# Performance work log

Hardware: AMD Instinct MI355X
Metric: run time of the kernel (lower is better)

Reference implementation:

```python
import jax, jax.numpy as jnp
import numpy as np

B, T, N, C = 32, 12, 1024, 64
NW = T - 3  # number of temporal windows / conv output length


def setup_inputs() -> dict:
    key = jax.random.key(0)
    ks = jax.random.split(key, 10)
    return {
        "data": jax.random.normal(ks[0], (B, T, N, C), jnp.float32),
        "adj": jax.random.uniform(ks[1], (4 * N, 4 * N), jnp.float32) / (4.0 * N),
        "temporal_emb": jax.random.normal(ks[2], (1, T, 1, C), jnp.float32) * 0.05,
        "spatial_emb": jax.random.normal(ks[3], (1, 1, N, C), jnp.float32) * 0.05,
        "conv_wl": jax.random.normal(ks[4], (C, C, 1, 2), jnp.float32) * 0.05,
        "conv_bl": jnp.zeros((C,), jnp.float32),
        "conv_wr": jax.random.normal(ks[5], (C, C, 1, 2), jnp.float32) * 0.05,
        "conv_br": jnp.zeros((C,), jnp.float32),
        "fc_w": jax.random.normal(ks[6], (NW, 3, C, 2 * C), jnp.float32) * 0.05,
        "fc_b": jnp.zeros((NW, 3, 2 * C), jnp.float32),
    }


def reference(data, adj, temporal_emb, spatial_emb, conv_wl, conv_bl, conv_wr, conv_br, fc_w, fc_b):
    Bs, Ts, Ns, Cs = data.shape
    nw = Ts - 3
    x = data + temporal_emb + spatial_emb  # [B,T,N,C]

    # Gated dilated temporal conv: Conv2d kernel (1,2), dilation (1,3) over time
    # out[b,t,n,o] = sum_c w[o,c,0,0]*x[b,t,n,c] + w[o,c,0,1]*x[b,t+3,n,c] + b[o]
    def dconv(w, b):
        return (jnp.einsum('btnc,oc->btno', x[:, :nw], w[:, :, 0, 0])
                + jnp.einsum('btnc,oc->btno', x[:, 3:], w[:, :, 0, 1]) + b)

    data_res = jax.nn.sigmoid(dconv(conv_wl, conv_bl)) * jnp.tanh(dconv(conv_wr, conv_br))  # [B,nw,N,C]

    # Sliding windows of 4 time steps -> [nw, B, 4N, C]
    wins = jnp.stack([x[:, i:i + 4].reshape(Bs, 4 * Ns, Cs) for i in range(nw)], axis=0)

    F = fc_w.shape[-1] // 2  # GLU filter size

    def stsgcm(xw, Ws, bs):
        # xw: [B,4N,C]; Ws: [3,Cin,2F]; bs: [3,2F]
        h = xw
        outs = []
        for k in range(Ws.shape[0]):
            h = jnp.einsum('vw,bwc->bvc', adj, h)       # graph aggregation
            g = h @ Ws[k] + bs[k]                        # linear
            h = g[..., :F] * jax.nn.sigmoid(g[..., F:])  # GLU
            outs.append(h[:, Ns:2 * Ns])                 # middle vertex block
        return jnp.max(jnp.stack(outs, axis=0), axis=0)  # [B,N,F]

    spatial = jax.vmap(stsgcm)(wins, fc_w, fc_b)  # [nw,B,N,F]
    return spatial.transpose(1, 0, 2, 3) + data_res
```

## Files before the change

### kernel.cpp

```cpp
#include <hip/hip_runtime.h>
#include <math.h>

typedef unsigned char  u8;
typedef unsigned short u16;
typedef unsigned int   u32;
typedef __attribute__((ext_vector_type(8))) short bf16x8;
typedef __attribute__((ext_vector_type(4))) float f32x4;

typedef const void __attribute__((address_space(1))) gv1_t;
typedef void       __attribute__((address_space(3))) lv3_t;
#define GLL(g, l) __builtin_amdgcn_global_load_lds((gv1_t*)(g), (lv3_t*)(l), 16, 0, 0)

__device__ __forceinline__ u16 f2b(float x) {
    union { float f; u32 u; } v; v.f = x;
    u32 r = v.u + 0x7FFFu + ((v.u >> 16) & 1u);
    return (u16)(r >> 16);
}
__device__ __forceinline__ float b2f(u32 x) {
    union { u32 u; float f; } v; v.u = x << 16;
    return v.f;
}
__device__ __forceinline__ float fast_sigmoid(float x) {
    return __builtin_amdgcn_rcpf(1.0f + __builtin_amdgcn_exp2f(-x * 1.44269504f));
}
__device__ __forceinline__ float fast_tanh(float x) {
    return 2.0f * __builtin_amdgcn_rcpf(1.0f + __builtin_amdgcn_exp2f(-x * 2.88539008f)) - 1.0f;
}

__device__ __forceinline__ u8 f2e4m3(float x) {
    union { float f; u32 u; } v; v.f = x;
    u32 s = (v.u >> 24) & 0x80u;
    u32 a = v.u & 0x7fffffffu;
    if (a >= 0x43d80000u) return (u8)(s | 0x7e);
    if (a >= 0x3c800000u) {
        u32 expf = a >> 23;
        u32 keep = (a >> 20) & 7u;
        u32 rest = a & 0xfffffu;
        u32 vv = ((expf - 120u) << 3) | keep;
        vv += (rest > 0x80000u) || ((rest == 0x80000u) && (keep & 1u));
        return (u8)(s | vv);
    }
    float t = fabsf(x) * 512.0f;
    u32 ti = (u32)(t + 0.5f);
    return (u8)(s | ti);
}
__device__ __forceinline__ float e4m3f(u32 b) {
    u32 e = (b >> 3) & 15u, m = b & 7u;
    union { u32 u; float f; } t;
    t.u = ((e + 120u) << 23) | (m << 20);
    float v = e ? t.f : ((float)m * 0.001953125f);
    return (b & 0x80u) ? -v : v;
}

__global__ void cvt_adj_fp8(const float* __restrict__ a, u8* __restrict__ o, int n) {
    for (int i = (blockIdx.x * 256 + threadIdx.x) * 4; i < n; i += gridDim.x * 256 * 4) {
        float4 v = *(const float4*)&a[i];
        u32 pk = (u32)f2e4m3(v.x * 8192.0f) | ((u32)f2e4m3(v.y * 8192.0f) << 8)
               | ((u32)f2e4m3(v.z * 8192.0f) << 16) | ((u32)f2e4m3(v.w * 8192.0f) << 24);
        *(u32*)&o[i] = pk;
    }
}

__global__ void prep_x(const float* __restrict__ data, const float* __restrict__ temb,
                       const float* __restrict__ semb, u16* __restrict__ Xn, u8* __restrict__ XT) {
    const int n0 = blockIdx.x * 64, t = blockIdx.y, b = blockIdx.z;
    const int tid = threadIdx.x;
    __shared__ u16 lt[64][66];
#pragma unroll
    for (int p = 0; p < 4; p++) {
        int n = p * 16 + (tid >> 4);
        int c = (tid & 15) * 4;
        size_t gi = ((size_t)(b * 12 + t) * 1024 + n0 + n) * 64 + c;
        float4 v  = *(const float4*)&data[gi];
        float4 tv = *(const float4*)&temb[t * 64 + c];
        float4 sv = *(const float4*)&semb[(n0 + n) * 64 + c];
        u16 u0 = f2b(v.x + tv.x + sv.x);
        u16 u1 = f2b(v.y + tv.y + sv.y);
        u16 u2 = f2b(v.z + tv.z + sv.z);
        u16 u3 = f2b(v.w + tv.w + sv.w);
        uint2 pk; pk.x = (u32)u0 | ((u32)u1 << 16); pk.y = (u32)u2 | ((u32)u3 << 16);
        *(uint2*)&Xn[gi] = pk;
        lt[n][c + 0] = u0; lt[n][c + 1] = u1; lt[n][c + 2] = u2; lt[n][c + 3] = u3;
    }
    __syncthreads();
    const int c = tid >> 2, q = tid & 3;
    u32 w[4];
#pragma unroll
    for (int i = 0; i < 4; i++) {
        u32 b0 = f2e4m3(b2f(lt[q * 16 + i * 4 + 0][c]));
        u32 b1 = f2e4m3(b2f(lt[q * 16 + i * 4 + 1][c]));
        u32 b2 = f2e4m3(b2f(lt[q * 16 + i * 4 + 2][c]));
        u32 b3 = f2e4m3(b2f(lt[q * 16 + i * 4 + 3][c]));
        w[i] = b0 | (b1 << 8) | (b2 << 16) | (b3 << 24);
    }
    size_t xo = ((size_t)(b * 64 + c)) * 12288 + (size_t)t * 1024 + n0 + q * 16;
    uint4 pk; pk.x = w[0]; pk.y = w[1]; pk.z = w[2]; pk.w = w[3];
    *(uint4*)&XT[xo] = pk;
}

__global__ void prep_w(const float* __restrict__ fcw, const float* __restrict__ cwl,
                       const float* __restrict__ cwr, u16* __restrict__ Wt, u16* __restrict__ Wc) {
    const int blk = blockIdx.x, tid = threadIdx.x;
    if (blk < 27) {
        const float* src = fcw + (size_t)blk * 64 * 128;
        u16* dst = Wt + (size_t)blk * 128 * 64;
        for (int e = tid; e < 8192; e += 256) {
            int c = e >> 7, f = e & 127;
            dst[f * 64 + c] = f2b(src[c * 128 + f]);
        }
    } else {
        for (int e = tid; e < 16384; e += 256) {
            int o = e >> 7, k = e & 127;
            float v = (o < 64) ? cwl[(o * 64 + (k & 63)) * 2 + (k >> 6)]
                               : cwr[((o - 64) * 64 + (k & 63)) * 2 + (k >> 6)];
            Wc[o * 128 + k] = f2b(v);
        }
    }
}

__global__ __launch_bounds__(256) void dconv_gemm(
    const u16* __restrict__ Xn, const u16* __restrict__ Wc,
    const float* __restrict__ cbl, const float* __restrict__ cbr,
    float* __restrict__ out) {
    const int n0 = blockIdx.x * 128, t = blockIdx.y, b = blockIdx.z;
    const int tid = threadIdx.x, lane = tid & 63, wid = tid >> 6;
    __shared__ u16 alds[2][128 * 32];
    const u16* base0 = Xn + (size_t)(b * 12 + t) * 1024 * 64;
    const u16* base3 = Xn + (size_t)(b * 12 + t + 3) * 1024 * 64;

    auto stage = [&](int buf, int kt) {
        int k0 = kt * 32;
#pragma unroll
        for (int q = 0; q < 2; q++) {
            int r = wid * 32 + q * 16 + (lane >> 2);
            int k = k0 + (lane & 3) * 8;
            const u16* gs = (k < 64) ? base0 + (size_t)(n0 + r) * 64 + k
                                     : base3 + (size_t)(n0 + r) * 64 + (k - 64);
            GLL(gs, &alds[buf][(wid * 32 + q * 16) * 32]);
        }
    };

    f32x4 acc[2][8] = {};
    stage(0, 0);
    __syncthreads();
    const int a_off = (wid * 32 + (lane & 15)) * 32 + (lane >> 4) * 8;
    for (int kt = 0; kt < 4; kt++) {
        int cur = kt & 1;
        if (kt < 3) stage(cur ^ 1, kt + 1);
        bf16x8 af[2];
#pragma unroll
        for (int m = 0; m < 2; m++) af[m] = *(const bf16x8*)&alds[cur][a_off + m * 16 * 32];
#pragma unroll
        for (int n = 0; n < 8; n++) {
            bf16x8 bq = *(const bf16x8*)&Wc[(n * 16 + (lane & 15)) * 128 + kt * 32 + (lane >> 4) * 8];
#pragma unroll
            for (int m = 0; m < 2; m++)
                acc[m][n] = __builtin_amdgcn_mfma_f32_16x16x32_bf16(af[m], bq, acc[m][n], 0, 0, 0);
        }
        __syncthreads();
    }
#pragma unroll
    for (int m = 0; m < 2; m++) {
#pragma unroll
        for (int n = 0; n < 4; n++) {
            int fp = n * 16 + (lane & 15);
            float b1 = cbl[fp], b2 = cbr[fp];
#pragma unroll
            for (int j = 0; j < 4; j++) {
                int row = wid * 32 + m * 16 + (lane >> 4) * 4 + j;
                float gl = acc[m][n][j] + b1;
                float gr = acc[m][n + 4][j] + b2;
                out[((size_t)(b * 9 + t) * 1024 + n0 + row) * 64 + fp] =
                    fast_sigmoid(gl) * fast_tanh(gr);
            }
        }
    }
}

#define SCB() __builtin_amdgcn_sched_barrier(0)
#define BARR() do { SCB(); __builtin_amdgcn_s_barrier(); SCB(); } while (0)
#define WAITK0 do { asm volatile("s_waitcnt lgkmcnt(0)" ::: "memory"); SCB(); } while (0)
#define GATE3 do { SCB(); asm volatile("s_waitcnt vmcnt(3)" ::: "memory"); SCB(); } while (0)
#define GATEZ do { SCB(); asm volatile("s_waitcnt vmcnt(0)" ::: "memory"); SCB(); } while (0)

template <int STAGE>
__global__ __launch_bounds__(512, 4) void agg_fp8(
    const u8* __restrict__ A, const u8* __restrict__ Bt,
    const u16* __restrict__ Wt, const float* __restrict__ fcb,
    u8* __restrict__ P, int win0, int vbase, int nout, int ks, float ysc) {
    const int tid = threadIdx.x, lane = tid & 63, wid = tid >> 6;
    const int wr = wid >> 1, wc = wid & 1;
    const int bx = blockIdx.x, by = blockIdx.y, z = blockIdx.z;
    const int rowBase = by * 256, colBase = bx * 128;
    const int win = win0 + z;
    __shared__ u8 ldsb[65536];
    __shared__ float biasSm[128];
    biasSm[tid & 127] = fcb[(win * 3 + ks) * 128 + (tid & 127)];
    const u8* Az = (STAGE == 0) ? (A + (size_t)win * 1024)
                                : (A + (size_t)z * 2048 * 4096);
    const size_t strideA = (STAGE == 0) ? 12288 : 4096;

    const int r_st = lane >> 2;
    const int sc_st = 16 * ((lane & 3) ^ ((r_st >> 1) & 3));
    auto stageA = [&](int buf, int s, int kt) {
        int r_l = s * 128 + wid * 16 + r_st;
        GLL(Az + (size_t)(rowBase + r_l) * strideA + kt * 64 + sc_st,
            &ldsb[buf * 24576 + (s * 128 + wid * 16) * 64]);
    };
    auto stageB = [&](int buf, int kt) {
        int r_l = wid * 16 + r_st;
        GLL(Bt + (size_t)(vbase + colBase + r_l) * 4096 + kt * 64 + sc_st,
            &ldsb[buf * 24576 + 16384 + (wid * 16) * 64]);
    };

    f32x4 acc[4][4] = {};
    long aF[4][2], bF[4][2];

#define RD_AB(buf)                                                            \
    _Pragma("unroll") for (int mm = 0; mm < 4; mm++)                          \
    _Pragma("unroll") for (int kk = 0; kk < 2; kk++) {                        \
        int r = wr * 64 + mm * 16 + (lane & 15);                              \
        int o = kk * 32 + (lane >> 4) * 8;                                    \
        int phys = (((o >> 4) ^ ((r >> 1) & 3)) << 4) + (o & 15);             \
        aF[mm][kk] = *(const long*)&ldsb[(buf) * 24576 + r * 64 + phys];      \
    }                                                                         \
    _Pragma("unroll") for (int nn = 0; nn < 4; nn++)                          \
    _Pragma("unroll") for (int kk = 0; kk < 2; kk++) {                        \
        int r = wc * 64 + nn * 16 + (lane & 15);                              \
        int o = kk * 32 + (lane >> 4) * 8;                                    \
        int phys = (((o >> 4) ^ ((r >> 1) & 3)) << 4) + (o & 15);             \
        bF[nn][kk] = *(const long*)&ldsb[(buf) * 24576 + 16384 + r * 64 + phys]; \
    }
#define MFMA32()                                                              \
    __builtin_amdgcn_s_setprio(1);                                            \
    _Pragma("unroll") for (int mm = 0; mm < 4; mm++)                          \
    _Pragma("unroll") for (int nn = 0; nn < 4; nn++)                          \
    _Pragma("unroll") for (int kk = 0; kk < 2; kk++)                          \
        acc[mm][nn] = __builtin_amdgcn_mfma_f32_16x16x32_fp8_fp8(             \
            aF[mm][kk], bF[nn][kk], acc[mm][nn], 0, 0, 0);                    \
    __builtin_amdgcn_s_setprio(0);

#define TILE11(RB, T2S) do {                                                  \
    BARR();                                                                   \
    RD_AB(RB);                                                                \
    WAITK0;                                                                   \
    BARR();                                                                   \
    stageA(RB, 0, T2S); stageA(RB, 1, T2S); stageB(RB, T2S);                  \
    SCB();                                                                    \
    MFMA32();                                                                 \
    GATE3;                                                                    \
} while (0)

    stageA(0, 0, 0); stageA(0, 1, 0); stageB(0, 0);
    stageA(1, 0, 1); stageA(1, 1, 1); stageB(1, 1);
    GATE3;

    for (int t = 0; t < 62; t += 2) {
        TILE11(0, t + 2);
        TILE11(1, t + 3);
    }
    BARR();
    RD_AB(0);
    WAITK0;
    BARR();
    MFMA32();
    GATEZ;
    BARR();
    RD_AB(1);
    WAITK0;
    MFMA32();

    __syncthreads();
    u16* YT = (u16*)ldsb;
#pragma unroll
    for (int mm = 0; mm < 4; mm++) {
        int c0 = mm * 16 + (lane >> 4) * 4;
#pragma unroll
        for (int nn = 0; nn < 4; nn++) {
            int v = wc * 64 + nn * 16 + (lane & 15);
            ushort4 pk;
            pk.x = f2b(acc[mm][nn][0] * ysc); pk.y = f2b(acc[mm][nn][1] * ysc);
            pk.z = f2b(acc[mm][nn][2] * ysc); pk.w = f2b(acc[mm][nn][3] * ysc);
            int addr = (wr * 128 + v) * 64 + (((c0 >> 3) ^ (v & 7)) << 3) + (c0 & 7);
            *(ushort4*)&YT[addr] = pk;
        }
    }
    __syncthreads();

    const int bat = wid >> 1, fh = wid & 1;
    const u16* Wl = Wt + (size_t)(win * 3 + ks) * 8192;
    u8* Pz = P + (size_t)z * 2048 * nout;
    bf16x8 aw[4][2];
#pragma unroll
    for (int p = 0; p < 4; p++) {
        int mt = (p & 1) + fh * 2 + (p >> 1) * 4;
#pragma unroll
        for (int kk = 0; kk < 2; kk++)
            aw[p][kk] = *(const bf16x8*)&Wl[(mt * 16 + (lane & 15)) * 64 + kk * 32 + (lane >> 4) * 8];
    }
#pragma unroll
    for (int vp = 0; vp < 4; vp++) {
        f32x4 acc2[4][2] = {};
        bf16x8 bq2[2][2];
#pragma unroll
        for (int nt = 0; nt < 2; nt++) {
            int v = vp * 32 + nt * 16 + (lane & 15);
#pragma unroll
            for (int kk = 0; kk < 2; kk++) {
                int ch = kk * 4 + (lane >> 4);
                bq2[nt][kk] = *(const bf16x8*)&YT[(bat * 128 + v) * 64 + ((ch ^ (v & 7)) << 3)];
            }
        }
#pragma unroll
        for (int p = 0; p < 4; p++)
#pragma unroll
            for (int nt = 0; nt < 2; nt++)
#pragma unroll
                for (int kk = 0; kk < 2; kk++)
                    acc2[p][nt] = __builtin_amdgcn_mfma_f32_16x16x32_bf16(
                        aw[p][kk], bq2[nt][kk], acc2[p][nt], 0, 0, 0);
#pragma unroll
        for (int p = 0; p < 2; p++) {
            int mt = (p & 1) + fh * 2;
#pragma unroll
            for (int j = 0; j < 4; j++) {
                int f = mt * 16 + (lane >> 4) * 4 + j;
                float b1 = biasSm[f], b2v = biasSm[f + 64];
#pragma unroll
                for (int nt = 0; nt < 2; nt++) {
                    float g1 = acc2[p][nt][j] + b1;
                    float g2 = acc2[p + 2][nt][j] + b2v;
                    float val = g1 * fast_sigmoid(g2);
                    int row = rowBase + bat * 64 + f;
                    int col = colBase + vp * 32 + nt * 16 + (lane & 15);
                    Pz[(size_t)row * nout + col] = f2e4m3(val * 512.0f);
                }
            }
        }
    }
#undef RD_AB
#undef MFMA32
#undef TILE11
}

__global__ void final_add(const u8* __restrict__ P1, const u8* __restrict__ P2,
                          const u8* __restrict__ P3, float* __restrict__ out, int win0) {
    const int n0 = blockIdx.x * 64, b = blockIdx.y, z = blockIdx.z;
    const int win = win0 + z;
    const int tid = threadIdx.x;
    __shared__ float tl[64][65];
    {
        int f = tid >> 2, q = tid & 3;
        size_t o12 = ((size_t)z * 2048 + b * 64 + f) * 4096 + 1024 + n0 + q * 16;
        size_t o3  = ((size_t)z * 2048 + b * 64 + f) * 1024 + n0 + q * 16;
        uint4 a  = *(const uint4*)&P1[o12];
        uint4 c2 = *(const uint4*)&P2[o12];
        uint4 d  = *(const uint4*)&P3[o3];
        const u32 aw[4] = {a.x, a.y, a.z, a.w};
        const u32 bw[4] = {c2.x, c2.y, c2.z, c2.w};
        const u32 dw[4] = {d.x, d.y, d.z, d.w};
#pragma unroll
        for (int w = 0; w < 4; w++)
#pragma unroll
            for (int j = 0; j < 4; j++) {
                float va = e4m3f((aw[w] >> (j * 8)) & 0xffu);
                float vb = e4m3f((bw[w] >> (j * 8)) & 0xffu);
                float vd = e4m3f((dw[w] >> (j * 8)) & 0xffu);
                tl[q * 16 + w * 4 + j][f] = fmaxf(fmaxf(va, vb), vd) * (1.0f / 512.0f);
            }
    }
    __syncthreads();
    {
        int n = tid >> 2, q = tid & 3;
        size_t oo = ((size_t)(b * 9 + win) * 1024 + n0 + n) * 64 + q * 16;
#pragma unroll
        for (int i = 0; i < 16; i += 4) {
            float4 cur = *(const float4*)&out[oo + i];
            cur.x += tl[n][q * 16 + i + 0];
            cur.y += tl[n][q * 16 + i + 1];
            cur.z += tl[n][q * 16 + i + 2];
            cur.w += tl[n][q * 16 + i + 3];
            *(float4*)&out[oo + i] = cur;
        }
    }
}

extern "C" void kernel_launch(void* const* d_in, const int* in_sizes, int n_in,
                              void* d_out, int out_size, void* d_ws, size_t ws_size,
                              hipStream_t stream) {
    const float* data = (const float*)d_in[0];
    const float* adj  = (const float*)d_in[1];
    const float* temb = (const float*)d_in[2];
    const float* semb = (const float*)d_in[3];
    const float* cwl  = (const float*)d_in[4];
    const float* cbl  = (const float*)d_in[5];
    const float* cwr  = (const float*)d_in[6];
    const float* cbr  = (const float*)d_in[7];
    const float* fcw  = (const float*)d_in[8];
    const float* fcb  = (const float*)d_in[9];
    float* out = (float*)d_out;

    const float YS1 = 1.0f / 8192.0f;
    const float YS2 = 1.0f / 4194304.0f;

    char* p = (char*)d_ws;
    auto alloc = [&](size_t bytes) -> char* {
        char* r = p;
        p += (bytes + 255) & ~(size_t)255;
        return r;
    };
    const size_t SZ_XT  = 2048UL * 12288;
    const size_t SZ_XN  = 32UL * 12 * 1024 * 64 * 2;
    const size_t SZ_ADJ = 4096UL * 4096;
    const size_t SZ_WT  = 27UL * 128 * 64 * 2;
    const size_t SZ_WC  = 128UL * 128 * 2;
    const size_t SZ_P12 = 2048UL * 4096;
    const size_t SZ_P3  = 2048UL * 1024;
    u8*  XT   = (u8*)alloc(SZ_XT);
    u8*  adjb = (u8*)alloc(SZ_ADJ);
    u16* Wt   = (u16*)alloc(SZ_WT);
    u16* Wc   = (u16*)alloc(SZ_WC);
    size_t fixed = (size_t)(p - (char*)d_ws);

    bool single = (fixed + 9 * (2 * SZ_P12) + SZ_XN + 1024 <= ws_size);
    if (single) {
        u8* P1 = (u8*)alloc(9 * SZ_P12);
        u8* P2 = (u8*)alloc(9 * SZ_P12);
        u8* P3 = XT;
        u16* Xn = (u16*)P2;

        cvt_adj_fp8<<<4096, 256, 0, stream>>>(adj, adjb, 4096 * 4096);
        prep_x<<<dim3(16, 12, 32), 256, 0, stream>>>(data, temb, semb, Xn, XT);
        prep_w<<<28, 256, 0, stream>>>(fcw, cwl, cwr, Wt, Wc);
        dconv_gemm<<<dim3(8, 9, 32), 256, 0, stream>>>(Xn, Wc, cbl, cbr, out);

        agg_fp8<0><<<dim3(32, 8, 9), 512, 0, stream>>>(XT, adjb, Wt, fcb, P1, 0, 0, 4096, 0, YS1);
        agg_fp8<1><<<dim3(32, 8, 9), 512, 0, stream>>>(P1, adjb, Wt, fcb, P2, 0, 0, 4096, 1, YS2);
        agg_fp8<1><<<dim3(8, 8, 9), 512, 0, stream>>>(P2, adjb, Wt, fcb, P3, 0, 1024, 1024, 2, YS2);
        final_add<<<dim3(16, 32, 9), 256, 0, stream>>>(P1, P2, P3, out, 0);
    } else {
        char* winBase = p;
        size_t avail = ws_size - (size_t)(winBase - (char*)d_ws);
        const size_t perwin = 2 * SZ_P12 + SZ_P3 + 3 * 256;
        int cap = (int)(avail / perwin);
        if (cap > 9) cap = 9;
        if (cap < 1) cap = 1;
        u8* P1 = (u8*)alloc((size_t)cap * SZ_P12);
        u8* P2 = (u8*)alloc((size_t)cap * SZ_P12);
        u8* P3 = (u8*)alloc((size_t)cap * SZ_P3);
        u16* Xn = ((size_t)cap * perwin >= SZ_XN + 256) ? (u16*)winBase : (u16*)alloc(SZ_XN);

        cvt_adj_fp8<<<4096, 256, 0, stream>>>(adj, adjb, 4096 * 4096);
        prep_x<<<dim3(16, 12, 32), 256, 0, stream>>>(data, temb, semb, Xn, XT);
        prep_w<<<28, 256, 0, stream>>>(fcw, cwl, cwr, Wt, Wc);
        dconv_gemm<<<dim3(8, 9, 32), 256, 0, stream>>>(Xn, Wc, cbl, cbr, out);

        int ngroups = (9 + cap - 1) / cap;
        int gbase = 9 / ngroups, grem = 9 % ngroups;
        int w0 = 0;
        for (int g = 0; g < ngroups; g++) {
            int cw = gbase + (g < grem ? 1 : 0);
            agg_fp8<0><<<dim3(32, 8, cw), 512, 0, stream>>>(XT, adjb, Wt, fcb, P1, w0, 0, 4096, 0, YS1);
            agg_fp8<1><<<dim3(32, 8, cw), 512, 0, stream>>>(P1, adjb, Wt, fcb, P2, w0, 0, 4096, 1, YS2);
            agg_fp8<1><<<dim3(8, 8, cw), 512, 0, stream>>>(P2, adjb, Wt, fcb, P3, w0, 1024, 1024, 2, YS2);
            final_add<<<dim3(16, 32, cw), 256, 0, stream>>>(P1, P2, P3, out, w0);
            w0 += cw;
        }
    }
}
```

Before: 1.186 ms.

## Pre-swizzle fp8 operands in global memory with 8-byte XOR granularity

Producers (adjacency conversion, XT prep, GLU epilogue) now write fp8 data into global memory with an 8-byte-chunk XOR swizzle keyed on the row. The aggregation GEMM can then stage tiles with plain, unswizzled global-to-LDS loads and read 8-byte fragments conflict-free through a 3-bit XOR. Before, the swizzle worked on 16-byte chunks, so the two 8-byte reads inside a chunk could still hit the same LDS banks. Consumers in final_add unswizzle on load, which costs extra index math and a conditional word permutation in several kernels.

```diff
diff --git a/kernel.cpp b/kernel.cpp
--- a/kernel.cpp
+++ b/kernel.cpp
@@ -52,12 +52,17 @@
     return (b & 0x80u) ? -v : v;
 }
 
+
 __global__ void cvt_adj_fp8(const float* __restrict__ a, u8* __restrict__ o, int n) {
     for (int i = (blockIdx.x * 256 + threadIdx.x) * 4; i < n; i += gridDim.x * 256 * 4) {
         float4 v = *(const float4*)&a[i];
         u32 pk = (u32)f2e4m3(v.x * 8192.0f) | ((u32)f2e4m3(v.y * 8192.0f) << 8)
                | ((u32)f2e4m3(v.z * 8192.0f) << 16) | ((u32)f2e4m3(v.w * 8192.0f) << 24);
-        *(u32*)&o[i] = pk;
+        int row = i >> 12;
+        int s8 = (row >> 1) & 7;
+        int k = i & 4095;
+        int addr = (i & ~63) | ((((k >> 3) & 7) ^ s8) << 3) | (k & 7);
+        *(u32*)&o[addr] = pk;
     }
 }
 
@@ -93,8 +98,13 @@
         u32 b3 = f2e4m3(b2f(lt[q * 16 + i * 4 + 3][c]));
         w[i] = b0 | (b1 << 8) | (b2 << 16) | (b3 << 24);
     }
-    size_t xo = ((size_t)(b * 64 + c)) * 12288 + (size_t)t * 1024 + n0 + q * 16;
-    uint4 pk; pk.x = w[0]; pk.y = w[1]; pk.z = w[2]; pk.w = w[3];
+    const int row = b * 64 + c;
+    const int s8 = (row >> 1) & 7;
+    const int p0 = ((2 * q) ^ s8) & 6;
+    uint4 pk;
+    if (s8 & 1) { pk.x = w[2]; pk.y = w[3]; pk.z = w[0]; pk.w = w[1]; }
+    else        { pk.x = w[0]; pk.y = w[1]; pk.z = w[2]; pk.w = w[3]; }
+    size_t xo = (size_t)row * 12288 + (size_t)t * 1024 + n0 + p0 * 8;
     *(uint4*)&XT[xo] = pk;
 }
 
@@ -201,15 +211,15 @@
     const size_t strideA = (STAGE == 0) ? 12288 : 4096;
 
     const int r_st = lane >> 2;
-    const int sc_st = 16 * ((lane & 3) ^ ((r_st >> 1) & 3));
+    const int c_st = (lane & 3) * 16;
     auto stageA = [&](int buf, int s, int kt) {
         int r_l = s * 128 + wid * 16 + r_st;
-        GLL(Az + (size_t)(rowBase + r_l) * strideA + kt * 64 + sc_st,
+        GLL(Az + (size_t)(rowBase + r_l) * strideA + kt * 64 + c_st,
             &ldsb[buf * 24576 + (s * 128 + wid * 16) * 64]);
     };
     auto stageB = [&](int buf, int kt) {
         int r_l = wid * 16 + r_st;
-        GLL(Bt + (size_t)(vbase + colBase + r_l) * 4096 + kt * 64 + sc_st,
+        GLL(Bt + (size_t)(vbase + colBase + r_l) * 4096 + kt * 64 + c_st,
             &ldsb[buf * 24576 + 16384 + (wid * 16) * 64]);
     };
 
@@ -220,15 +230,15 @@
     _Pragma("unroll") for (int mm = 0; mm < 4; mm++)                          \
     _Pragma("unroll") for (int kk = 0; kk < 2; kk++) {                        \
         int r = wr * 64 + mm * 16 + (lane & 15);                              \
-        int o = kk * 32 + (lane >> 4) * 8;                                    \
-        int phys = (((o >> 4) ^ ((r >> 1) & 3)) << 4) + (o & 15);             \
+        int o8 = kk * 4 + (lane >> 4);                                        \
+        int phys = (o8 ^ ((r >> 1) & 7)) << 3;                                \
         aF[mm][kk] = *(const long*)&ldsb[(buf) * 24576 + r * 64 + phys];      \
     }                                                                         \
     _Pragma("unroll") for (int nn = 0; nn < 4; nn++)                          \
     _Pragma("unroll") for (int kk = 0; kk < 2; kk++) {                        \
         int r = wc * 64 + nn * 16 + (lane & 15);                              \
-        int o = kk * 32 + (lane >> 4) * 8;                                    \
-        int phys = (((o >> 4) ^ ((r >> 1) & 3)) << 4) + (o & 15);             \
+        int o8 = kk * 4 + (lane >> 4);                                        \
+        int phys = (o8 ^ ((r >> 1) & 7)) << 3;                                \
         bF[nn][kk] = *(const long*)&ldsb[(buf) * 24576 + 16384 + r * 64 + phys]; \
     }
 #define MFMA32()                                                              \
@@ -240,7 +250,7 @@
             aF[mm][kk], bF[nn][kk], acc[mm][nn], 0, 0, 0);                    \
     __builtin_amdgcn_s_setprio(0);
 
-#define TILE11(RB, T2S) do {                                                  \
+#define TILE12(RB, T2S) do {                                                  \
     BARR();                                                                   \
     RD_AB(RB);                                                                \
     WAITK0;                                                                   \
@@ -256,8 +266,8 @@
     GATE3;
 
     for (int t = 0; t < 62; t += 2) {
-        TILE11(0, t + 2);
-        TILE11(1, t + 3);
+        TILE12(0, t + 2);
+        TILE12(1, t + 3);
     }
     BARR();
     RD_AB(0);
@@ -326,21 +336,30 @@
             for (int j = 0; j < 4; j++) {
                 int f = mt * 16 + (lane >> 4) * 4 + j;
                 float b1 = biasSm[f], b2v = biasSm[f + 64];
+                int row = rowBase + bat * 64 + f;
+                int s8r = (row >> 1) & 7;
 #pragma unroll
                 for (int nt = 0; nt < 2; nt++) {
                     float g1 = acc2[p][nt][j] + b1;
                     float g2 = acc2[p + 2][nt][j] + b2v;
                     float val = g1 * fast_sigmoid(g2);
-                    int row = rowBase + bat * 64 + f;
-                    int col = colBase + vp * 32 + nt * 16 + (lane & 15);
-                    Pz[(size_t)row * nout + col] = f2e4m3(val * 512.0f);
+                    int colg = colBase + vp * 32 + nt * 16 + (lane & 15);
+                    int off = ((((colg >> 3) & 7) ^ s8r) << 3) | (colg & 7);
+                    Pz[(size_t)row * nout + (colg & ~63) + off] = f2e4m3(val * 512.0f);
                 }
             }
         }
     }
 #undef RD_AB
 #undef MFMA32
-#undef TILE11
+#undef TILE12
+}
+
+__device__ __forceinline__ uint4 ld_swz(const u8* p, size_t segBase, int q, int s8) {
+    int p0 = ((2 * q) ^ s8) & 6;
+    uint4 a = *(const uint4*)&p[segBase + p0 * 8];
+    if (s8 & 1) { u32 t0 = a.x, t1 = a.y; a.x = a.z; a.y = a.w; a.z = t0; a.w = t1; }
+    return a;
 }
 
 __global__ void final_add(const u8* __restrict__ P1, const u8* __restrict__ P2,
@@ -351,11 +370,13 @@
     __shared__ float tl[64][65];
     {
         int f = tid >> 2, q = tid & 3;
-        size_t o12 = ((size_t)z * 2048 + b * 64 + f) * 4096 + 1024 + n0 + q * 16;
-        size_t o3  = ((size_t)z * 2048 + b * 64 + f) * 1024 + n0 + q * 16;
-        uint4 a  = *(const uint4*)&P1[o12];
-        uint4 c2 = *(const uint4*)&P2[o12];
-        uint4 d  = *(const uint4*)&P3[o3];
+        int row = b * 64 + f;
+        int s8 = (row >> 1) & 7;
+        size_t seg12 = ((size_t)z * 2048 + row) * 4096 + 1024 + n0;
+        size_t seg3  = ((size_t)z * 2048 + row) * 1024 + n0;
+        uint4 a  = ld_swz(P1, seg12, q, s8);
+        uint4 c2 = ld_swz(P2, seg12, q, s8);
+        uint4 d  = ld_swz(P3, seg3, q, s8);
         const u32 aw[4] = {a.x, a.y, a.z, a.w};
         const u32 bw[4] = {c2.x, c2.y, c2.z, c2.w};
         const u32 dw[4] = {d.x, d.y, d.z, d.w};
```

Measured after the change: 1.169 ms. No clear change (-1.4%).

## Switch graph aggregation GEMMs to MX fp8 16x16x128 MFMA with pre-swizzled operands

Applied to the files above, without the earlier changes.

Replaces the fp8 16x16x32 MFMA aggregation kernel with one built on the gfx950 scaled 16x16x128 f8f6f4 MFMA, using 128-byte K tiles, 256-thread blocks and 128-row tiles. The adjacency, XT and intermediate P buffers are now written in global memory with an XOR-swizzled 16-byte chunk layout, so direct global-to-LDS loads arrive already bank-conflict-free. final_add reads through the same swizzle. The aim is higher MFMA throughput and fewer loop iterations; the cost is a smaller block tile that may lower operand reuse, plus more complex addressing everywhere.

```diff
diff --git a/kernel.cpp b/kernel.cpp
--- a/kernel.cpp
+++ b/kernel.cpp
@@ -5,6 +5,7 @@
 typedef unsigned short u16;
 typedef unsigned int   u32;
 typedef __attribute__((ext_vector_type(8))) short bf16x8;
+typedef __attribute__((ext_vector_type(8))) int   i32x8;
 typedef __attribute__((ext_vector_type(4))) float f32x4;
 
 typedef const void __attribute__((address_space(1))) gv1_t;
@@ -52,12 +53,15 @@
     return (b & 0x80u) ? -v : v;
 }
 
+
 __global__ void cvt_adj_fp8(const float* __restrict__ a, u8* __restrict__ o, int n) {
     for (int i = (blockIdx.x * 256 + threadIdx.x) * 4; i < n; i += gridDim.x * 256 * 4) {
         float4 v = *(const float4*)&a[i];
         u32 pk = (u32)f2e4m3(v.x * 8192.0f) | ((u32)f2e4m3(v.y * 8192.0f) << 8)
                | ((u32)f2e4m3(v.z * 8192.0f) << 16) | ((u32)f2e4m3(v.w * 8192.0f) << 24);
-        *(u32*)&o[i] = pk;
+        int row = i >> 12;
+        int addr = (i & ~127) | (((((i >> 4) & 7) ^ (row & 7)) << 4)) | (i & 15);
+        *(u32*)&o[addr] = pk;
     }
 }
 
@@ -93,9 +97,12 @@
         u32 b3 = f2e4m3(b2f(lt[q * 16 + i * 4 + 3][c]));
         w[i] = b0 | (b1 << 8) | (b2 << 16) | (b3 << 24);
     }
-    size_t xo = ((size_t)(b * 64 + c)) * 12288 + (size_t)t * 1024 + n0 + q * 16;
+    const int row = b * 64 + c;
+    size_t kk = (size_t)t * 1024 + n0 + q * 16;
+    size_t seg = kk & ~(size_t)127;
+    int chunk = (((int)(kk >> 4) & 7) ^ (row & 7));
     uint4 pk; pk.x = w[0]; pk.y = w[1]; pk.z = w[2]; pk.w = w[3];
-    *(uint4*)&XT[xo] = pk;
+    *(uint4*)&XT[(size_t)row * 12288 + seg + chunk * 16] = pk;
 }
 
 __global__ void prep_w(const float* __restrict__ fcw, const float* __restrict__ cwl,
@@ -180,18 +187,18 @@
 #define SCB() __builtin_amdgcn_sched_barrier(0)
 #define BARR() do { SCB(); __builtin_amdgcn_s_barrier(); SCB(); } while (0)
 #define WAITK0 do { asm volatile("s_waitcnt lgkmcnt(0)" ::: "memory"); SCB(); } while (0)
-#define GATE3 do { SCB(); asm volatile("s_waitcnt vmcnt(3)" ::: "memory"); SCB(); } while (0)
+#define GATE8 do { SCB(); asm volatile("s_waitcnt vmcnt(8)" ::: "memory"); SCB(); } while (0)
 #define GATEZ do { SCB(); asm volatile("s_waitcnt vmcnt(0)" ::: "memory"); SCB(); } while (0)
 
 template <int STAGE>
-__global__ __launch_bounds__(512, 4) void agg_fp8(
+__global__ __launch_bounds__(256, 2) void agg_mx(
     const u8* __restrict__ A, const u8* __restrict__ Bt,
     const u16* __restrict__ Wt, const float* __restrict__ fcb,
     u8* __restrict__ P, int win0, int vbase, int nout, int ks, float ysc) {
     const int tid = threadIdx.x, lane = tid & 63, wid = tid >> 6;
     const int wr = wid >> 1, wc = wid & 1;
     const int bx = blockIdx.x, by = blockIdx.y, z = blockIdx.z;
-    const int rowBase = by * 256, colBase = bx * 128;
+    const int rowBase = by * 128, colBase = bx * 128;
     const int win = win0 + z;
     __shared__ u8 ldsb[65536];
     __shared__ float biasSm[128];
@@ -200,75 +207,79 @@
                                 : (A + (size_t)z * 2048 * 4096);
     const size_t strideA = (STAGE == 0) ? 12288 : 4096;
 
-    const int r_st = lane >> 2;
-    const int sc_st = 16 * ((lane & 3) ^ ((r_st >> 1) & 3));
+    const int r8  = lane >> 3;
+    const int c16 = (lane & 7) * 16;
     auto stageA = [&](int buf, int s, int kt) {
-        int r_l = s * 128 + wid * 16 + r_st;
-        GLL(Az + (size_t)(rowBase + r_l) * strideA + kt * 64 + sc_st,
-            &ldsb[buf * 24576 + (s * 128 + wid * 16) * 64]);
+        int r_l = s * 32 + wid * 8;
+        GLL(Az + (size_t)(rowBase + r_l + r8) * strideA + (size_t)kt * 128 + c16,
+            &ldsb[buf * 32768 + r_l * 128]);
     };
-    auto stageB = [&](int buf, int kt) {
-        int r_l = wid * 16 + r_st;
-        GLL(Bt + (size_t)(vbase + colBase + r_l) * 4096 + kt * 64 + sc_st,
-            &ldsb[buf * 24576 + 16384 + (wid * 16) * 64]);
+    auto stageB = [&](int buf, int s, int kt) {
+        int r_l = s * 32 + wid * 8;
+        GLL(Bt + (size_t)(vbase + colBase + r_l + r8) * 4096 + (size_t)kt * 128 + c16,
+            &ldsb[buf * 32768 + 16384 + r_l * 128]);
     };
+#define STAGE8(buf, kt) do { stageA(buf, 0, kt); stageA(buf, 1, kt); \
+                             stageA(buf, 2, kt); stageA(buf, 3, kt); \
+                             stageB(buf, 0, kt); stageB(buf, 1, kt); \
+                             stageB(buf, 2, kt); stageB(buf, 3, kt); } while (0)
 
     f32x4 acc[4][4] = {};
-    long aF[4][2], bF[4][2];
+    i32x8 fa[4], fb[4];
+    const int q0 = lane >> 4;
 
 #define RD_AB(buf)                                                            \
-    _Pragma("unroll") for (int mm = 0; mm < 4; mm++)                          \
-    _Pragma("unroll") for (int kk = 0; kk < 2; kk++) {                        \
+    _Pragma("unroll") for (int mm = 0; mm < 4; mm++) {                        \
         int r = wr * 64 + mm * 16 + (lane & 15);                              \
-        int o = kk * 32 + (lane >> 4) * 8;                                    \
-        int phys = (((o >> 4) ^ ((r >> 1) & 3)) << 4) + (o & 15);             \
-        aF[mm][kk] = *(const long*)&ldsb[(buf) * 24576 + r * 64 + phys];      \
+        int h = r & 7;                                                        \
+        const u8* bp = &ldsb[(buf) * 32768 + r * 128];                        \
+        ((uint4*)&fa[mm])[0] = *(const uint4*)&bp[((2 * q0) ^ h) * 16];       \
+        ((uint4*)&fa[mm])[1] = *(const uint4*)&bp[((2 * q0 + 1) ^ h) * 16];   \
     }                                                                         \
-    _Pragma("unroll") for (int nn = 0; nn < 4; nn++)                          \
-    _Pragma("unroll") for (int kk = 0; kk < 2; kk++) {                        \
+    _Pragma("unroll") for (int nn = 0; nn < 4; nn++) {                        \
         int r = wc * 64 + nn * 16 + (lane & 15);                              \
-        int o = kk * 32 + (lane >> 4) * 8;                                    \
-        int phys = (((o >> 4) ^ ((r >> 1) & 3)) << 4) + (o & 15);             \
-        bF[nn][kk] = *(const long*)&ldsb[(buf) * 24576 + 16384 + r * 64 + phys]; \
-    }
-#define MFMA32()                                                              \
+        int h = r & 7;                                                        \
+        const u8* bp = &ldsb[(buf) * 32768 + 16384 + r * 128];                \
+        ((uint4*)&fb[nn])[0] = *(const uint4*)&bp[((2 * q0) ^ h) * 16];       \
+        ((uint4*)&fb[nn])[1] = *(const uint4*)&bp[((2 * q0 + 1) ^ h) * 16];   \
+    }
+#define MFMA16()                                                              \
     __builtin_amdgcn_s_setprio(1);                                            \
     _Pragma("unroll") for (int mm = 0; mm < 4; mm++)                          \
     _Pragma("unroll") for (int nn = 0; nn < 4; nn++)                          \
-    _Pragma("unroll") for (int kk = 0; kk < 2; kk++)                          \
-        acc[mm][nn] = __builtin_amdgcn_mfma_f32_16x16x32_fp8_fp8(             \
-            aF[mm][kk], bF[nn][kk], acc[mm][nn], 0, 0, 0);                    \
+        acc[mm][nn] = __builtin_amdgcn_mfma_scale_f32_16x16x128_f8f6f4(       \
+            fa[mm], fb[nn], acc[mm][nn], 0, 0, 0, 127, 0, 127);               \
     __builtin_amdgcn_s_setprio(0);
 
-#define TILE11(RB, T2S) do {                                                  \
+#define TILE14(RB, T2S) do {                                                  \
     BARR();                                                                   \
     RD_AB(RB);                                                                \
     WAITK0;                                                                   \
     BARR();                                                                   \
-    stageA(RB, 0, T2S); stageA(RB, 1, T2S); stageB(RB, T2S);                  \
+    STAGE8(RB, T2S);                                                          \
     SCB();                                                                    \
-    MFMA32();                                                                 \
-    GATE3;                                                                    \
+    MFMA16();                                                                 \
+    GATE8;                                                                    \
 } while (0)
 
-    stageA(0, 0, 0); stageA(0, 1, 0); stageB(0, 0);
-    stageA(1, 0, 1); stageA(1, 1, 1); stageB(1, 1);
-    GATE3;
-
-    for (int t = 0; t < 62; t += 2) {
-        TILE11(0, t + 2);
-        TILE11(1, t + 3);
+    STAGE8(0, 0);
+    STAGE8(1, 1);
+    GATE8;
+
+    for (int t = 0; t < 30; t += 2) {
+        TILE14(0, t + 2);
+        TILE14(1, t + 3);
     }
     BARR();
     RD_AB(0);
     WAITK0;
     BARR();
-    MFMA32();
+    MFMA16();
     GATEZ;
     BARR();
     RD_AB(1);
     WAITK0;
-    MFMA32();
+    MFMA16();
 
     __syncthreads();
     u16* YT = (u16*)ldsb;
@@ -326,21 +337,31 @@
             for (int j = 0; j < 4; j++) {
                 int f = mt * 16 + (lane >> 4) * 4 + j;
                 float b1 = biasSm[f], b2v = biasSm[f + 64];
+                int row = rowBase + bat * 64 + f;
 #pragma unroll
                 for (int nt = 0; nt < 2; nt++) {
                     float g1 = acc2[p][nt][j] + b1;
                     float g2 = acc2[p + 2][nt][j] + b2v;
                     float val = g1 * fast_sigmoid(g2);
-                    int row = rowBase + bat * 64 + f;
-                    int col = colBase + vp * 32 + nt * 16 + (lane & 15);
-                    Pz[(size_t)row * nout + col] = f2e4m3(val * 512.0f);
+                    int colg = colBase + vp * 32 + nt * 16 + (lane & 15);
+                    int seg = colg & ~127;
+                    int chunk = (((colg >> 4) & 7) ^ (row & 7));
+                    Pz[(size_t)row * nout + seg + chunk * 16 + (colg & 15)] =
+                        f2e4m3(val * 512.0f);
                 }
             }
         }
     }
 #undef RD_AB
-#undef MFMA32
-#undef TILE11
+#undef MFMA16
+#undef TILE14
+#undef STAGE8
+}
+
+__device__ __forceinline__ uint4 ld_swz(const u8* p, size_t rowBytes, size_t k, int h) {
+    size_t seg = k & ~(size_t)127;
+    int chunk = ((int)(k >> 4) & 7) ^ h;
+    return *(const uint4*)&p[rowBytes + seg + chunk * 16];
 }
 
 __global__ void final_add(const u8* __restrict__ P1, const u8* __restrict__ P2,
@@ -351,11 +372,13 @@
     __shared__ float tl[64][65];
     {
         int f = tid >> 2, q = tid & 3;
-        size_t o12 = ((size_t)z * 2048 + b * 64 + f) * 4096 + 1024 + n0 + q * 16;
-        size_t o3  = ((size_t)z * 2048 + b * 64 + f) * 1024 + n0 + q * 16;
-        uint4 a  = *(const uint4*)&P1[o12];
-        uint4 c2 = *(const uint4*)&P2[o12];
-        uint4 d  = *(const uint4*)&P3[o3];
+        int row = b * 64 + f;
+        int h = row & 7;
+        size_t rb12 = ((size_t)z * 2048 + row) * 4096;
+        size_t rb3  = ((size_t)z * 2048 + row) * 1024;
+        uint4 a  = ld_swz(P1, rb12, (size_t)1024 + n0 + q * 16, h);
+        uint4 c2 = ld_swz(P2, rb12, (size_t)1024 + n0 + q * 16, h);
+        uint4 d  = ld_swz(P3, rb3, (size_t)n0 + q * 16, h);
         const u32 aw[4] = {a.x, a.y, a.z, a.w};
         const u32 bw[4] = {c2.x, c2.y, c2.z, c2.w};
         const u32 dw[4] = {d.x, d.y, d.z, d.w};
@@ -434,9 +457,9 @@
         prep_w<<<28, 256, 0, stream>>>(fcw, cwl, cwr, Wt, Wc);
         dconv_gemm<<<dim3(8, 9, 32), 256, 0, stream>>>(Xn, Wc, cbl, cbr, out);
 
-        agg_fp8<0><<<dim3(32, 8, 9), 512, 0, stream>>>(XT, adjb, Wt, fcb, P1, 0, 0, 4096, 0, YS1);
-        agg_fp8<1><<<dim3(32, 8, 9), 512, 0, stream>>>(P1, adjb, Wt, fcb, P2, 0, 0, 4096, 1, YS2);
-        agg_fp8<1><<<dim3(8, 8, 9), 512, 0, stream>>>(P2, adjb, Wt, fcb, P3, 0, 1024, 1024, 2, YS2);
+        agg_mx<0><<<dim3(32, 16, 9), 256, 0, stream>>>(XT, adjb, Wt, fcb, P1, 0, 0, 4096, 0, YS1);
+        agg_mx<1><<<dim3(32, 16, 9), 256, 0, stream>>>(P1, adjb, Wt, fcb, P2, 0, 0, 4096, 1, YS2);
+        agg_mx<1><<<dim3(8, 16, 9), 256, 0, stream>>>(P2, adjb, Wt, fcb, P3, 0, 1024, 1024, 2, YS2);
         final_add<<<dim3(16, 32, 9), 256, 0, stream>>>(P1, P2, P3, out, 0);
     } else {
         char* winBase = p;
@@ -460,9 +483,9 @@
         int w0 = 0;
         for (int g = 0; g < ngroups; g++) {
             int cw = gbase + (g < grem ? 1 : 0);
-            agg_fp8<0><<<dim3(32, 8, cw), 512, 0, stream>>>(XT, adjb, Wt, fcb, P1, w0, 0, 4096, 0, YS1);
-            agg_fp8<1><<<dim3(32, 8, cw), 512, 0, stream>>>(P1, adjb, Wt, fcb, P2, w0, 0, 4096, 1, YS2);
-            agg_fp8<1><<<dim3(8, 8, cw), 512, 0, stream>>>(P2, adjb, Wt, fcb, P3, w0, 1024, 1024, 2, YS2);
+            agg_mx<0><<<dim3(32, 16, cw), 256, 0, stream>>>(XT, adjb, Wt, fcb, P1, w0, 0, 4096, 0, YS1);
+            agg_mx<1><<<dim3(32, 16, cw), 256, 0, stream>>>(P1, adjb, Wt, fcb, P2, w0, 0, 4096, 1, YS2);
+            agg_mx<1><<<dim3(8, 16, cw), 256, 0, stream>>>(P2, adjb, Wt, fcb, P3, w0, 1024, 1024, 2, YS2);
             final_add<<<dim3(16, 32, cw), 256, 0, stream>>>(P1, P2, P3, out, w0);
             w0 += cw;
         }
```

Result: faster. 1.017 ms (-14.2%).
